# Kernel tuning notes

Measured on AMD Instinct MI355X. Metric: run time of the kernel, lower is better.

## Reference

```python
import jax, jax.numpy as jnp
import numpy as np

N_NODES = 100000


def _gcn_conv(x, W, b, src, dst, n):
    # PyG GCNConv (default): add self-loops, norm = deg^{-1/2}[src] * deg^{-1/2}[dst]
    # degree computed on target nodes (col) with unit edge weights, then
    # out[i] = sum_{(j->i)} norm_ji * (x_j @ W) + b
    loops = jnp.arange(n, dtype=src.dtype)
    s = jnp.concatenate([src, loops])
    d = jnp.concatenate([dst, loops])
    deg = jax.ops.segment_sum(jnp.ones_like(d, dtype=x.dtype), d, num_segments=n)
    dinv = jnp.where(deg > 0, jax.lax.rsqrt(deg), 0.0)
    h = x @ W                                  # [n, out_dim]
    norm = (dinv[s] * dinv[d])[:, None]        # [E+n, 1]
    msg = h[s] * norm                          # gather + scale
    out = jax.ops.segment_sum(msg, d, num_segments=n)  # scatter-add to targets
    return out + b


def setup_inputs() -> dict:
    key = jax.random.key(0)
    ks = jax.random.split(key, 4)
    x = jax.random.normal(ks[0], (N_NODES, 128), dtype=jnp.float32)
    edge_index = jax.random.randint(ks[1], (2, 1600000), 0, N_NODES, dtype=jnp.int64)
    W1 = jax.random.normal(ks[2], (128, 16), dtype=jnp.float32) * (1.0 / np.sqrt(128))
    b1 = jnp.zeros((16,), dtype=jnp.float32)
    W2 = jax.random.normal(ks[3], (16, 3), dtype=jnp.float32) * (1.0 / np.sqrt(16))
    b2 = jnp.zeros((3,), dtype=jnp.float32)
    return {"x": x, "edge_index": edge_index, "W1": W1, "b1": b1, "W2": W2, "b2": b2}


def reference(x, edge_index, W1, b1, W2, b2):
    src, dst = edge_index[0], edge_index[1]
    n = x.shape[0]
    h = _gcn_conv(x, W1, b1, src, dst, n)
    h = jax.nn.relu(h)
    # F.dropout in eval mode == identity (deterministic baseline)
    h = _gcn_conv(h, W2, b2, src, dst, n)
    return jax.nn.log_softmax(h, axis=1)
```

## Files before the change

kernel.cpp:

```cpp
#include <hip/hip_runtime.h>
#include <hip/hip_fp16.h>
#include <math.h>


#define BSH 9
#define BNODES 512
#define P1 512
#define GROWS 64
#define K2BUF 10240
#define BCAP 12288
#define EPT 16
#define EPT2 12
#define CSTR 16

struct alignas(8) Half4 { __half x, y, z, w; };

__global__ void k1b_fat(const int* __restrict__ src, const int* __restrict__ dst,
                        int* __restrict__ cursor,
                        unsigned int* __restrict__ staging,
                        const float* __restrict__ x, const float* __restrict__ W1,
                        Half4* __restrict__ g1h, int NBK, int n, int E) {
    __shared__ float sx[GROWS * 132];
    __shared__ float4 sW4[512];
    int b = blockIdx.x;
    if (b < P1) {
        int* hist  = (int*)sx;
        int* cs    = hist + 256;
        int* rbase = hist + 512;
        int* cur   = hist + 768;
        int* buf   = hist + 1024;
        int* gaddr = buf + 3200;
        int t = threadIdx.x;
        hist[t] = 0; cur[t] = 0;
        __syncthreads();
        int slice = (E + P1 - 1) / P1;
        int e0 = b * slice, e1 = min(E, e0 + slice);
        int len = e1 - e0;
        int dl[EPT], sl[EPT];
        int cnt = 0;
        for (int e = e0 + t; e < e1 && cnt < EPT; e += 256, ++cnt) {
            dl[cnt] = dst[e];
            sl[cnt] = src[e];
        }
        for (int i = 0; i < cnt; ++i)
            atomicAdd(&hist[dl[i] >> BSH], 1);
        __syncthreads();
        int h = hist[t];
        cs[t] = h;
        __syncthreads();
        for (int o = 1; o < 256; o <<= 1) {
            int add = (t >= o) ? cs[t - o] : 0;
            __syncthreads();
            cs[t] += add;
            __syncthreads();
        }
        int incl = cs[t];
        __syncthreads();
        cs[t] = incl - h;
        rbase[t] = (h > 0 && t < NBK) ? atomicAdd(&cursor[t * CSTR], h) : 0;
        __syncthreads();
        for (int i = 0; i < cnt; ++i) {
            int d = dl[i], s = sl[i];
            int k = d >> BSH;
            int tk = atomicAdd(&cur[k], 1);
            int pos = cs[k] + tk;
            buf[pos] = (s << BSH) | (d & (BNODES - 1));
            int g = rbase[k] + tk;
            gaddr[pos] = (g < BCAP) ? (k * BCAP + g) : -1;
        }
        __syncthreads();
        for (int p = t; p < len; p += 256) {
            int a = gaddr[p];
            if (a >= 0) staging[a] = (unsigned int)buf[p];
        }
    } else {
        int t = threadIdx.x;
        int base = (b - P1) * GROWS;
        for (int i = t; i < 512; i += 256) sW4[i] = ((const float4*)W1)[i];
        for (int i = t; i < GROWS * 32; i += 256) {
            int r = i >> 5, c = i & 31;
            int row = base + r;
            float4 v = (row < n) ? ((const float4*)x)[(size_t)row * 32 + c]
                                 : make_float4(0.f, 0.f, 0.f, 0.f);
            *((float4*)&sx[r * 132 + c * 4]) = v;
        }
        __syncthreads();
        int r = t >> 2, c4 = t & 3;
        int row = base + r;
        if (row >= n) return;
        float4 acc = make_float4(0.f, 0.f, 0.f, 0.f);
        #pragma unroll 8
        for (int q = 0; q < 32; ++q) {
            float4 xv = *((const float4*)&sx[r * 132 + q * 4]);
            #pragma unroll
            for (int j = 0; j < 4; ++j) {
                float s = (j == 0) ? xv.x : (j == 1) ? xv.y : (j == 2) ? xv.z : xv.w;
                float4 w = sW4[(q * 4 + j) * 4 + c4];
                acc.x += s * w.x; acc.y += s * w.y; acc.z += s * w.z; acc.w += s * w.w;
            }
        }
        Half4 hh;
        hh.x = __float2half(acc.x); hh.y = __float2half(acc.y);
        hh.z = __float2half(acc.z); hh.w = __float2half(acc.w);
        g1h[(size_t)row * 4 + c4] = hh;
    }
}

__global__ void __launch_bounds__(1024) k2_bucket(
        const unsigned int* __restrict__ staging, const int* __restrict__ cursor,
        int* __restrict__ csr, int* __restrict__ deg, float* __restrict__ dinv,
        int* __restrict__ row_start, Half4* __restrict__ g1h, int n) {
    __shared__ int lh[BNODES], sc[BNODES], lcur[BNODES];
    __shared__ float ldv[BNODES];
    __shared__ int buf[K2BUF];
    int kb = blockIdx.x, t = threadIdx.x;
    int node0 = kb << BSH;
    int nloc = min(BNODES, n - node0);
    int ebase = kb * BCAP;
    int ecnt = min(cursor[kb * CSTR], BCAP);
    if (t < BNODES) { lh[t] = 0; lcur[t] = 0; }
    __syncthreads();
    int el[EPT2];
    int cnt = 0;
    for (int e = t; e < ecnt && cnt < EPT2; e += 1024, ++cnt)
        el[cnt] = (int)staging[ebase + e];
    for (int i = 0; i < cnt; ++i)
        atomicAdd(&lh[el[i] & (BNODES - 1)], 1);
    __syncthreads();
    int own = 0;
    if (t < BNODES) { own = lh[t]; sc[t] = own; }
    __syncthreads();
    for (int o = 1; o < BNODES; o <<= 1) {
        int add = 0;
        if (t < BNODES && t >= o) add = sc[t - o];
        __syncthreads();
        if (t < BNODES) sc[t] += add;
        __syncthreads();
    }
    if (t < BNODES) {
        int excl = sc[t] - own;
        if (t < nloc) {
            deg[node0 + t] = own;
            row_start[node0 + t] = ebase + excl;
            float dv = rsqrtf((float)(own + 1));
            dinv[node0 + t] = dv;
            ldv[t] = dv;
        }
        sc[t] = excl;
    }
    __syncthreads();
    if (ecnt <= K2BUF) {
        for (int i = 0; i < cnt; ++i) {
            int p = el[i];
            int loc = p & (BNODES - 1);
            int tk = atomicAdd(&lcur[loc], 1);
            buf[sc[loc] + tk] = p >> BSH;
        }
        __syncthreads();
        for (int p = t; p < ecnt; p += 1024)
            csr[ebase + p] = buf[p];
    } else {
        for (int i = 0; i < cnt; ++i) {
            int p = el[i];
            int loc = p & (BNODES - 1);
            int tk = atomicAdd(&lcur[loc], 1);
            csr[ebase + sc[loc] + tk] = p >> BSH;
        }
    }
    for (int j = t; j < nloc * 4; j += 1024) {
        float dv = ldv[j >> 2];
        Half4 v = g1h[(size_t)node0 * 4 + j];
        v.x = __float2half(__half2float(v.x) * dv);
        v.y = __float2half(__half2float(v.y) * dv);
        v.z = __float2half(__half2float(v.z) * dv);
        v.w = __float2half(__half2float(v.w) * dv);
        g1h[(size_t)node0 * 4 + j] = v;
    }
}

__global__ void k_gather1(const uint4* __restrict__ g1q, const int* __restrict__ csr,
                          const int* __restrict__ row_start, const int* __restrict__ deg,
                          const float* __restrict__ dinv, const float* __restrict__ b1,
                          const float* __restrict__ W2, Half4* __restrict__ g2h, int n) {
    int idx = blockIdx.x * 256 + threadIdx.x;
    int i = idx >> 4, l = idx & 15;
    if (i >= n) return;
    int off = row_start[i], dg = deg[i];
    float acc[16];
    #pragma unroll
    for (int j = 0; j < 16; ++j) acc[j] = 0.f;
    if (l == 0) {
        uint4 p0 = g1q[2 * (size_t)i], p1 = g1q[2 * (size_t)i + 1];
        const __half2* h0 = reinterpret_cast<const __half2*>(&p0);
        const __half2* h1 = reinterpret_cast<const __half2*>(&p1);
        #pragma unroll
        for (int j = 0; j < 4; ++j) {
            float2 f0 = __half22float2(h0[j]);
            float2 f1 = __half22float2(h1[j]);
            acc[2 * j] += f0.x; acc[2 * j + 1] += f0.y;
            acc[8 + 2 * j] += f1.x; acc[9 + 2 * j] += f1.y;
        }
    }
    for (int k = l; k < dg; k += 16) {
        int s = csr[off + k];
        uint4 p0 = g1q[2 * (size_t)s], p1 = g1q[2 * (size_t)s + 1];
        const __half2* h0 = reinterpret_cast<const __half2*>(&p0);
        const __half2* h1 = reinterpret_cast<const __half2*>(&p1);
        #pragma unroll
        for (int j = 0; j < 4; ++j) {
            float2 f0 = __half22float2(h0[j]);
            float2 f1 = __half22float2(h1[j]);
            acc[2 * j] += f0.x; acc[2 * j + 1] += f0.y;
            acc[8 + 2 * j] += f1.x; acc[9 + 2 * j] += f1.y;
        }
    }
    #pragma unroll
    for (int j = 0; j < 8; ++j) {
        float send = (l & 1) ? acc[j] : acc[j + 8];
        float recv = __shfl_xor(send, 1);
        acc[j] = ((l & 1) ? acc[j + 8] : acc[j]) + recv;
    }
    #pragma unroll
    for (int j = 0; j < 4; ++j) {
        float send = (l & 2) ? acc[j] : acc[j + 4];
        float recv = __shfl_xor(send, 2);
        acc[j] = ((l & 2) ? acc[j + 4] : acc[j]) + recv;
    }
    #pragma unroll
    for (int j = 0; j < 2; ++j) {
        float send = (l & 4) ? acc[j] : acc[j + 2];
        float recv = __shfl_xor(send, 4);
        acc[j] = ((l & 4) ? acc[j + 2] : acc[j]) + recv;
    }
    {
        float send = (l & 8) ? acc[0] : acc[1];
        float recv = __shfl_xor(send, 8);
        acc[0] = ((l & 8) ? acc[1] : acc[0]) + recv;
    }
    int f = ((l & 1) << 3) | ((l & 2) << 1) | ((l & 4) >> 1) | ((l & 8) >> 3);
    float di = dinv[i];
    float z = fmaxf(0.f, di * acc[0] + b1[f]);
    float o0 = z * W2[f * 3 + 0];
    float o1 = z * W2[f * 3 + 1];
    float o2 = z * W2[f * 3 + 2];
    #pragma unroll
    for (int m = 1; m < 16; m <<= 1) {
        o0 += __shfl_xor(o0, m);
        o1 += __shfl_xor(o1, m);
        o2 += __shfl_xor(o2, m);
    }
    if (l != 0) return;
    Half4 g;
    g.x = __float2half(di * o0); g.y = __float2half(di * o1);
    g.z = __float2half(di * o2); g.w = __float2half(0.f);
    g2h[i] = g;
}

__global__ void k_gather2(const Half4* __restrict__ g2h, const int* __restrict__ csr,
                          const int* __restrict__ row_start, const int* __restrict__ deg,
                          const float* __restrict__ dinv, const float* __restrict__ b2,
                          float* __restrict__ out, int n) {
    int idx = blockIdx.x * 256 + threadIdx.x;
    int i = idx >> 4, l = idx & 15;
    if (i >= n) return;
    int off = row_start[i], dg = deg[i];
    float v0 = 0.f, v1 = 0.f, v2 = 0.f;
    if (l == 0) {
        Half4 s = g2h[i];
        v0 = __half2float(s.x); v1 = __half2float(s.y); v2 = __half2float(s.z);
    }
    for (int e = l; e < dg; e += 16) {
        int s = csr[off + e];
        Half4 g = g2h[s];
        v0 += __half2float(g.x); v1 += __half2float(g.y); v2 += __half2float(g.z);
    }
    #pragma unroll
    for (int o = 1; o < 16; o <<= 1) {
        v0 += __shfl_xor(v0, o);
        v1 += __shfl_xor(v1, o);
        v2 += __shfl_xor(v2, o);
    }
    if (l >= 3) return;
    float di = dinv[i];
    float a0 = di * v0 + b2[0];
    float a1 = di * v1 + b2[1];
    float a2 = di * v2 + b2[2];
    float m = fmaxf(a0, fmaxf(a1, a2));
    float lse = logf(expf(a0 - m) + expf(a1 - m) + expf(a2 - m));
    float r = (l == 0) ? a0 : (l == 1) ? a1 : a2;
    out[(size_t)i * 3 + l] = r - m - lse;
}

extern "C" void kernel_launch(void* const* d_in, const int* in_sizes, int n_in,
                              void* d_out, int out_size, void* d_ws, size_t ws_size,
                              hipStream_t stream) {
    const float* x  = (const float*)d_in[0];
    const int*   ei = (const int*)d_in[1];
    const float* W1 = (const float*)d_in[2];
    const float* b1 = (const float*)d_in[3];
    const float* W2 = (const float*)d_in[4];
    const float* b2 = (const float*)d_in[5];
    float* out = (float*)d_out;

    const int n = in_sizes[0] / 128;
    const int E = in_sizes[1] / 2;
    const int* src = ei;
    const int* dst = ei + E;

    const int NBK = (n + BNODES - 1) >> BSH;

    auto align = [](size_t v) { return (v + 255) & ~(size_t)255; };
    char* ws = (char*)d_ws;
    size_t o = 0;
    int* cursor   = (int*)(ws + o); o = align(o + (size_t)NBK * CSTR * 4);
    int* deg      = (int*)(ws + o); o = align(o + (size_t)n * 4);
    float* dinv   = (float*)(ws + o); o = align(o + (size_t)n * 4);
    int* row_start= (int*)(ws + o); o = align(o + (size_t)n * 4);
    unsigned int* staging = (unsigned int*)(ws + o); o = align(o + (size_t)NBK * BCAP * 4);
    int* csr      = (int*)(ws + o); o = align(o + (size_t)NBK * BCAP * 4);
    Half4* g1h    = (Half4*)(ws + o); o = align(o + (size_t)n * 4 * 8);
    Half4* g2h    = (Half4*)(ws + o); o = align(o + (size_t)n * 8);

    const int B = 256;
    int gGemm = (n + GROWS - 1) / GROWS;
    int gn16  = (16 * n + B - 1) / B;

    hipMemsetAsync(cursor, 0, (size_t)NBK * CSTR * 4, stream);
    k1b_fat<<<P1 + gGemm, B, 0, stream>>>(src, dst, cursor, staging,
                                          x, W1, g1h, NBK, n, E);
    k2_bucket<<<NBK, 1024, 0, stream>>>(staging, cursor, csr, deg, dinv, row_start, g1h, n);
    k_gather1<<<gn16, B, 0, stream>>>((const uint4*)g1h, csr, row_start, deg, dinv, b1, W2,
                                      g2h, n);
    k_gather2<<<gn16, B, 0, stream>>>(g2h, csr, row_start, deg, dinv, b2, out, n);
}
```

Measured before the change: 166.8 us.

## Use wavefront shuffle scans and direct-load GEMM with cross-lane reduction

Replaces the shared-memory Hillis-Steele prefix scans in both the edge-bucketing block and the k2 bucket kernel with wavefront shuffle scans plus a small per-wave sum combine, cutting many block-wide barriers. The x@W1 path no longer stages x rows in LDS. Each of the four lanes per row now loads a strided quarter of the row directly from global memory, computes partial sums for all 16 outputs, and reduces across lanes with xor shuffles. This cuts LDS traffic and the shared footprint, but adds more registers and shuffle work per thread.

Result: no change. 163.6 us (-1.9%).

```diff
diff --git a/kernel.cpp b/kernel.cpp
--- a/kernel.cpp
+++ b/kernel.cpp
@@ -20,17 +20,17 @@
                         unsigned int* __restrict__ staging,
                         const float* __restrict__ x, const float* __restrict__ W1,
                         Half4* __restrict__ g1h, int NBK, int n, int E) {
-    __shared__ float sx[GROWS * 132];
-    __shared__ float4 sW4[512];
+    __shared__ int smem[7432];
     int b = blockIdx.x;
+    int t = threadIdx.x;
     if (b < P1) {
-        int* hist  = (int*)sx;
-        int* cs    = hist + 256;
-        int* rbase = hist + 512;
-        int* cur   = hist + 768;
-        int* buf   = hist + 1024;
-        int* gaddr = buf + 3200;
-        int t = threadIdx.x;
+        int* hist  = smem;
+        int* cs    = smem + 256;
+        int* rbase = smem + 512;
+        int* cur   = smem + 768;
+        int* buf   = smem + 1024;
+        int* gaddr = smem + 4224;
+        int* wsum  = smem + 7424;
         hist[t] = 0; cur[t] = 0;
         __syncthreads();
         int slice = (E + P1 - 1) / P1;
@@ -46,17 +46,19 @@
             atomicAdd(&hist[dl[i] >> BSH], 1);
         __syncthreads();
         int h = hist[t];
-        cs[t] = h;
-        __syncthreads();
-        for (int o = 1; o < 256; o <<= 1) {
-            int add = (t >= o) ? cs[t - o] : 0;
-            __syncthreads();
-            cs[t] += add;
-            __syncthreads();
-        }
-        int incl = cs[t];
-        __syncthreads();
-        cs[t] = incl - h;
+        int xx = h;
+        #pragma unroll
+        for (int o = 1; o < 64; o <<= 1) {
+            int v = __shfl_up(xx, o);
+            if ((t & 63) >= o) xx += v;
+        }
+        if ((t & 63) == 63) wsum[t >> 6] = xx;
+        __syncthreads();
+        int wv = t >> 6;
+        #pragma unroll
+        for (int i = 0; i < 4; ++i)
+            if (i < wv) xx += wsum[i];
+        cs[t] = xx - h;
         rbase[t] = (h > 0 && t < NBK) ? atomicAdd(&cursor[t * CSTR], h) : 0;
         __syncthreads();
         for (int i = 0; i < cnt; ++i) {
@@ -74,35 +76,48 @@
             if (a >= 0) staging[a] = (unsigned int)buf[p];
         }
     } else {
-        int t = threadIdx.x;
-        int base = (b - P1) * GROWS;
+        float4* sW4 = (float4*)smem;
         for (int i = t; i < 512; i += 256) sW4[i] = ((const float4*)W1)[i];
-        for (int i = t; i < GROWS * 32; i += 256) {
-            int r = i >> 5, c = i & 31;
-            int row = base + r;
-            float4 v = (row < n) ? ((const float4*)x)[(size_t)row * 32 + c]
-                                 : make_float4(0.f, 0.f, 0.f, 0.f);
-            *((float4*)&sx[r * 132 + c * 4]) = v;
-        }
         __syncthreads();
         int r = t >> 2, c4 = t & 3;
-        int row = base + r;
+        int row = (b - P1) * GROWS + r;
         if (row >= n) return;
-        float4 acc = make_float4(0.f, 0.f, 0.f, 0.f);
-        #pragma unroll 8
-        for (int q = 0; q < 32; ++q) {
-            float4 xv = *((const float4*)&sx[r * 132 + q * 4]);
+        float acc[16];
+        #pragma unroll
+        for (int j = 0; j < 16; ++j) acc[j] = 0.f;
+        const float4* xr = (const float4*)(x + (size_t)row * 128);
+        #pragma unroll
+        for (int q = 0; q < 8; ++q) {
+            float4 xv = xr[q * 4 + c4];
             #pragma unroll
             for (int j = 0; j < 4; ++j) {
+                int k = q * 16 + c4 * 4 + j;
                 float s = (j == 0) ? xv.x : (j == 1) ? xv.y : (j == 2) ? xv.z : xv.w;
-                float4 w = sW4[(q * 4 + j) * 4 + c4];
-                acc.x += s * w.x; acc.y += s * w.y; acc.z += s * w.z; acc.w += s * w.w;
+                #pragma unroll
+                for (int cq = 0; cq < 4; ++cq) {
+                    float4 w = sW4[k * 4 + cq];
+                    acc[cq * 4 + 0] += s * w.x; acc[cq * 4 + 1] += s * w.y;
+                    acc[cq * 4 + 2] += s * w.z; acc[cq * 4 + 3] += s * w.w;
+                }
             }
         }
+        #pragma unroll
+        for (int j = 0; j < 8; ++j) {
+            float send = (c4 & 1) ? acc[j] : acc[j + 8];
+            float recv = __shfl_xor(send, 1);
+            acc[j] = ((c4 & 1) ? acc[j + 8] : acc[j]) + recv;
+        }
+        #pragma unroll
+        for (int j = 0; j < 4; ++j) {
+            float send = (c4 & 2) ? acc[j] : acc[j + 4];
+            float recv = __shfl_xor(send, 2);
+            acc[j] = ((c4 & 2) ? acc[j + 4] : acc[j]) + recv;
+        }
+        int cidx = 2 * (c4 & 1) + ((c4 & 2) >> 1);
         Half4 hh;
-        hh.x = __float2half(acc.x); hh.y = __float2half(acc.y);
-        hh.z = __float2half(acc.z); hh.w = __float2half(acc.w);
-        g1h[(size_t)row * 4 + c4] = hh;
+        hh.x = __float2half(acc[0]); hh.y = __float2half(acc[1]);
+        hh.z = __float2half(acc[2]); hh.w = __float2half(acc[3]);
+        g1h[(size_t)row * 4 + cidx] = hh;
     }
 }
 
@@ -110,7 +125,7 @@
         const unsigned int* __restrict__ staging, const int* __restrict__ cursor,
         int* __restrict__ csr, int* __restrict__ deg, float* __restrict__ dinv,
         int* __restrict__ row_start, Half4* __restrict__ g1h, int n) {
-    __shared__ int lh[BNODES], sc[BNODES], lcur[BNODES];
+    __shared__ int lh[BNODES], sc[BNODES], lcur[BNODES], wsum[8];
     __shared__ float ldv[BNODES];
     __shared__ int buf[K2BUF];
     int kb = blockIdx.x, t = threadIdx.x;
@@ -127,18 +142,21 @@
     for (int i = 0; i < cnt; ++i)
         atomicAdd(&lh[el[i] & (BNODES - 1)], 1);
     __syncthreads();
-    int own = 0;
-    if (t < BNODES) { own = lh[t]; sc[t] = own; }
+    int own = (t < BNODES) ? lh[t] : 0;
+    int xx = own;
+    #pragma unroll
+    for (int o = 1; o < 64; o <<= 1) {
+        int v = __shfl_up(xx, o);
+        if ((t & 63) >= o) xx += v;
+    }
+    if (t < BNODES && (t & 63) == 63) wsum[t >> 6] = xx;
     __syncthreads();
-    for (int o = 1; o < BNODES; o <<= 1) {
-        int add = 0;
-        if (t < BNODES && t >= o) add = sc[t - o];
-        __syncthreads();
-        if (t < BNODES) sc[t] += add;
-        __syncthreads();
-    }
     if (t < BNODES) {
-        int excl = sc[t] - own;
+        int wv = t >> 6;
+        #pragma unroll
+        for (int i = 0; i < 8; ++i)
+            if (i < wv) xx += wsum[i];
+        int excl = xx - own;
         if (t < nloc) {
             deg[node0 + t] = own;
             row_start[node0 + t] = ebase + excl;
```
